# Performance work log

Hardware: AMD Instinct MI355X
Metric: run time of the kernel (lower is better)

Reference implementation:

```python
import jax, jax.numpy as jnp
import numpy as np

MARGIN = 1.0
EPS = 1e-12


def setup_inputs() -> dict:
    key = jax.random.key(0)
    k1, k2 = jax.random.split(key)
    embeddings = jax.random.normal(k1, (4096, 768), dtype=jnp.float32)
    labels = jax.random.randint(k2, (4096,), 0, 4, dtype=jnp.int64)
    return {"embeddings": embeddings, "labels": labels}


def reference(embeddings, labels):
    # F.normalize(p=2, dim=1): x / max(||x||, eps)
    norm = jnp.linalg.norm(embeddings, axis=1, keepdims=True)
    e = embeddings / jnp.maximum(norm, EPS)

    # Euclidean pairwise distance matrix (not squared)
    dot = e @ e.T                                  # [N, N]
    sq = jnp.diagonal(dot)                         # [N]
    dist = sq[None, :] - 2.0 * dot + sq[:, None]
    dist = jnp.sqrt(jnp.maximum(dist, 0.0) + EPS)  # [N, N]

    # Masks: positives = same label, off-diagonal; negatives = different label
    n = labels.shape[0]
    eq = labels[None, :] == labels[:, None]
    pos_mask = eq & ~jnp.eye(n, dtype=bool)
    neg_mask = ~eq

    # Batch-hard mining: per-anchor hardest positive (masked max) and
    # hardest negative (masked min) -- replaces the per-row Python loop.
    d_ap = jnp.max(jnp.where(pos_mask, dist, -jnp.inf), axis=1)  # [N]
    d_an = jnp.min(jnp.where(neg_mask, dist, jnp.inf), axis=1)   # [N]

    valid = jnp.any(pos_mask, axis=1)  # anchors with at least one positive
    per_anchor = jnp.maximum(d_ap - d_an + MARGIN, 0.0)
    per_anchor = jnp.where(valid, per_anchor, 0.0)
    n_valid = jnp.maximum(jnp.sum(valid.astype(jnp.float32)), 1.0)
    return jnp.sum(per_anchor) / n_valid
```

## Files before the change

### kernel.cpp

```cpp
#include <hip/hip_runtime.h>
#include <math.h>

#define N 4096
#define D 768
#define MARGIN 1.0f
#define NBLK 576

typedef _Float16 half8 __attribute__((ext_vector_type(8)));
typedef _Float16 half4 __attribute__((ext_vector_type(4)));
typedef float f32x4 __attribute__((ext_vector_type(4)));

__device__ __forceinline__ void gl2lds16(const void* g, void* l) {
    __builtin_amdgcn_global_load_lds((const __attribute__((address_space(1))) void*)g,
                                     (__attribute__((address_space(3))) void*)l, 16, 0, 0);
}

__global__ __launch_bounds__(256) void normalize_kernel(const float* __restrict__ x,
                                                        _Float16* __restrict__ e,
                                                        float* __restrict__ sq,
                                                        unsigned* __restrict__ ap_bits,
                                                        unsigned* __restrict__ an_bits,
                                                        unsigned* __restrict__ counter) {
    const int tid = threadIdx.x;
    const int wave = tid >> 6, lane = tid & 63;
    const int row = blockIdx.x * 4 + wave;

    const float4* xr = (const float4*)(x + (size_t)row * D);
    float4 f0 = xr[lane];
    float4 f1 = xr[lane + 64];
    float4 f2 = xr[lane + 128];

    float s = f0.x*f0.x + f0.y*f0.y + f0.z*f0.z + f0.w*f0.w
            + f1.x*f1.x + f1.y*f1.y + f1.z*f1.z + f1.w*f1.w
            + f2.x*f2.x + f2.y*f2.y + f2.z*f2.z + f2.w*f2.w;
    #pragma unroll
    for (int off = 1; off < 64; off <<= 1) s += __shfl_xor(s, off, 64);

    float scale = 1.0f / fmaxf(sqrtf(s), 1e-12f);

    half4* er = (half4*)(e + (size_t)row * D);
    half4 h0 = { (_Float16)(f0.x*scale), (_Float16)(f0.y*scale), (_Float16)(f0.z*scale), (_Float16)(f0.w*scale) };
    half4 h1 = { (_Float16)(f1.x*scale), (_Float16)(f1.y*scale), (_Float16)(f1.z*scale), (_Float16)(f1.w*scale) };
    half4 h2 = { (_Float16)(f2.x*scale), (_Float16)(f2.y*scale), (_Float16)(f2.z*scale), (_Float16)(f2.w*scale) };
    er[lane]       = h0;
    er[lane + 64]  = h1;
    er[lane + 128] = h2;

    if (lane == 0) {
        sq[row] = s * scale * scale;
        ap_bits[row] = 0u;
        an_bits[row] = 0x7f800000u;
    }
    if (blockIdx.x == 0 && tid == 0) *counter = 0u;
}

template<int MTN, int NTN, int BROWS>
__device__ __forceinline__ void tile_work(const _Float16* __restrict__ e,
                                          const float* __restrict__ sq,
                                          const int* __restrict__ labels,
                                          unsigned* __restrict__ ap_bits,
                                          unsigned* __restrict__ an_bits,
                                          unsigned short* S,
                                          int i0, int jbase,
                                          int wi, int wjL,
                                          int tid, int w, int lane, bool diag) {
    const int ln15 = lane & 15;
    const int lq   = lane >> 4;

    f32x4 acc[MTN][NTN] = {};

    for (int kt = 0; kt < 24; ++kt) {
        const int k0 = kt * 32;
        __syncthreads();
        #pragma unroll
        for (int p = 0; p < 2; ++p) {
            int s  = p * 256 + tid;
            int r  = s >> 2;
            int kg = (s & 3) ^ ((r >> 1) & 3);
            gl2lds16(e + (size_t)(i0 + r) * D + k0 + kg * 8,
                     (char*)S + (p * 256 + w * 64) * 16);
        }
        if constexpr (BROWS == 128) {
            #pragma unroll
            for (int p = 0; p < 2; ++p) {
                int s  = p * 256 + tid;
                int r  = s >> 2;
                int kg = (s & 3) ^ ((r >> 1) & 3);
                gl2lds16(e + (size_t)(jbase + r) * D + k0 + kg * 8,
                         (char*)S + 8192 + (p * 256 + w * 64) * 16);
            }
        } else {
            if (w < 2) {
                int s  = tid;
                int r  = s >> 2;
                int kg = (s & 3) ^ ((r >> 1) & 3);
                gl2lds16(e + (size_t)(jbase + r) * D + k0 + kg * 8,
                         (char*)S + 8192 + (w * 64) * 16);
            }
        }
        __syncthreads();

        half8 af[MTN], bf[NTN];
        #pragma unroll
        for (int mt = 0; mt < MTN; ++mt) {
            int r  = wi + mt * 16 + ln15;
            int kx = lq ^ ((r >> 1) & 3);
            af[mt] = *(const half8*)&S[r * 32 + kx * 8];
        }
        #pragma unroll
        for (int nt = 0; nt < NTN; ++nt) {
            int r  = wjL + nt * 16 + ln15;
            int kx = lq ^ ((r >> 1) & 3);
            bf[nt] = *(const half8*)&S[4096 + r * 32 + kx * 8];
        }
        #pragma unroll
        for (int mt = 0; mt < MTN; ++mt)
            #pragma unroll
            for (int nt = 0; nt < NTN; ++nt)
                acc[mt][nt] = __builtin_amdgcn_mfma_f32_16x16x32_f16(af[mt], bf[nt], acc[mt][nt], 0, 0, 0);
    }

    float sqi[MTN][4]; int labi[MTN][4];
    #pragma unroll
    for (int mt = 0; mt < MTN; ++mt)
        #pragma unroll
        for (int rg = 0; rg < 4; ++rg) {
            int i = i0 + wi + mt * 16 + lq * 4 + rg;
            sqi[mt][rg] = sq[i];
            labi[mt][rg] = labels[i];
        }
    float sqj[NTN]; int labj[NTN];
    #pragma unroll
    for (int nt = 0; nt < NTN; ++nt) {
        int j = jbase + wjL + nt * 16 + ln15;
        sqj[nt] = sq[j];
        labj[nt] = labels[j];
    }

    float api[MTN][4], ani[MTN][4], apj[NTN], anj[NTN];
    #pragma unroll
    for (int mt = 0; mt < MTN; ++mt)
        #pragma unroll
        for (int rg = 0; rg < 4; ++rg) { api[mt][rg] = -INFINITY; ani[mt][rg] = INFINITY; }
    #pragma unroll
    for (int nt = 0; nt < NTN; ++nt) { apj[nt] = -INFINITY; anj[nt] = INFINITY; }

    #pragma unroll
    for (int nt = 0; nt < NTN; ++nt) {
        int j = jbase + wjL + nt * 16 + ln15;
        #pragma unroll
        for (int mt = 0; mt < MTN; ++mt)
            #pragma unroll
            for (int rg = 0; rg < 4; ++rg) {
                int i = i0 + wi + mt * 16 + lq * 4 + rg;
                float d2 = sqi[mt][rg] + sqj[nt] - 2.0f * acc[mt][nt][rg];
                float dist = sqrtf(fmaxf(d2, 0.0f) + 1e-12f);
                if (labi[mt][rg] == labj[nt]) {
                    if (i != j) {
                        api[mt][rg] = fmaxf(api[mt][rg], dist);
                        apj[nt]     = fmaxf(apj[nt], dist);
                    }
                } else {
                    ani[mt][rg] = fminf(ani[mt][rg], dist);
                    anj[nt]     = fminf(anj[nt], dist);
                }
            }
    }

    #pragma unroll
    for (int mt = 0; mt < MTN; ++mt)
        #pragma unroll
        for (int rg = 0; rg < 4; ++rg) {
            float a_ = api[mt][rg], n_ = ani[mt][rg];
            #pragma unroll
            for (int off = 1; off < 16; off <<= 1) {
                a_ = fmaxf(a_, __shfl_xor(a_, off, 64));
                n_ = fminf(n_, __shfl_xor(n_, off, 64));
            }
            if (ln15 == 0) {
                int i = i0 + wi + mt * 16 + lq * 4 + rg;
                if (a_ > -1.0e37f) atomicMax(&ap_bits[i], __float_as_uint(a_));
                if (n_ <  1.0e37f) atomicMin(&an_bits[i], __float_as_uint(n_));
            }
        }

    if (!diag) {
        #pragma unroll
        for (int nt = 0; nt < NTN; ++nt) {
            float a_ = apj[nt], n_ = anj[nt];
            #pragma unroll
            for (int off = 16; off < 64; off <<= 1) {
                a_ = fmaxf(a_, __shfl_xor(a_, off, 64));
                n_ = fminf(n_, __shfl_xor(n_, off, 64));
            }
            if (lq == 0) {
                int j = jbase + wjL + nt * 16 + ln15;
                if (a_ > -1.0e37f) atomicMax(&ap_bits[j], __float_as_uint(a_));
                if (n_ <  1.0e37f) atomicMin(&an_bits[j], __float_as_uint(n_));
            }
        }
    }
}

__global__ __launch_bounds__(256) void mine_kernel(const _Float16* __restrict__ e,
                                                   const float* __restrict__ sq,
                                                   const int* __restrict__ labels,
                                                   unsigned* __restrict__ ap_bits,
                                                   unsigned* __restrict__ an_bits,
                                                   unsigned* __restrict__ counter,
                                                   float* __restrict__ out) {
    __shared__ unsigned short S[8192];

    const int tid  = threadIdx.x;
    const int w    = tid >> 6;
    const int lane = tid & 63;

    int t, jlo, small;
    if (blockIdx.x < 512) { t = blockIdx.x; jlo = 0; small = 0; }
    else { int s2 = blockIdx.x - 512; t = 512 + (s2 >> 2); jlo = (s2 & 3) * 32; small = 1; }

    int bi = 0, rem = t;
    while (rem >= 32 - bi) { rem -= 32 - bi; ++bi; }
    const int bj = bi + rem;
    const int i0 = bi * 128, j0 = bj * 128;

    if (!small)
        tile_work<4, 4, 128>(e, sq, labels, ap_bits, an_bits, S, i0, j0,
                             (w & 1) * 64, (w >> 1) * 64, tid, w, lane, bi == bj);
    else
        tile_work<2, 2, 32>(e, sq, labels, ap_bits, an_bits, S, i0, j0 + jlo,
                            w * 32, 0, tid, w, lane, bi == bj);

    __shared__ unsigned lastFlag;
    __syncthreads();
    if (tid == 0) {
        __builtin_amdgcn_fence(__ATOMIC_RELEASE, "agent");
        lastFlag = (atomicAdd(counter, 1u) == NBLK - 1) ? 1u : 0u;
    }
    __syncthreads();
    if (!lastFlag) return;
    __builtin_amdgcn_fence(__ATOMIC_ACQUIRE, "agent");

    __shared__ int cnt[4];
    __shared__ float red[8];
    if (tid < 4) cnt[tid] = 0;
    __syncthreads();
    int local[4] = {0, 0, 0, 0};
    for (int i = tid; i < N; i += 256) local[labels[i] & 3]++;
    #pragma unroll
    for (int c = 0; c < 4; c++) atomicAdd(&cnt[c], local[c]);
    __syncthreads();

    float sum = 0.f, nv = 0.f;
    for (int i = tid; i < N; i += 256) {
        int l = labels[i] & 3;
        if (cnt[l] >= 2) {
            nv += 1.f;
            float apv = __uint_as_float(ap_bits[i]);
            float anv = __uint_as_float(an_bits[i]);
            if (anv < 3.0e38f) sum += fmaxf(apv - anv + MARGIN, 0.f);
        }
    }

    #pragma unroll
    for (int off = 32; off; off >>= 1) {
        sum += __shfl_down(sum, off, 64);
        nv  += __shfl_down(nv,  off, 64);
    }
    if ((tid & 63) == 0) { red[tid >> 6] = sum; red[4 + (tid >> 6)] = nv; }
    __syncthreads();
    if (tid == 0) {
        float s = red[0] + red[1] + red[2] + red[3];
        float n = red[4] + red[5] + red[6] + red[7];
        out[0] = s / fmaxf(n, 1.f);
    }
}

extern "C" void kernel_launch(void* const* d_in, const int* in_sizes, int n_in,
                              void* d_out, int out_size, void* d_ws, size_t ws_size,
                              hipStream_t stream) {
    const float* x = (const float*)d_in[0];
    const int* labels = (const int*)d_in[1];
    float* out = (float*)d_out;

    _Float16* e = (_Float16*)d_ws;
    float* sq = (float*)(e + (size_t)N * D);
    unsigned* ap_bits = (unsigned*)(sq + N);
    unsigned* an_bits = ap_bits + N;
    unsigned* counter = an_bits + N;

    normalize_kernel<<<N / 4, 256, 0, stream>>>(x, e, sq, ap_bits, an_bits, counter);
    mine_kernel<<<NBLK, 256, 0, stream>>>(e, sq, labels, ap_bits, an_bits, counter, out);
}
```

Baseline: 127.3 us.

## Triple-buffer LDS K-tiles with async prefetch and remap blocks across XCDs

Replaces the single-buffered load-then-compute K loop with a three-stage LDS ring. Tiles are prefetched two steps ahead using global_load_lds, and explicit vmcnt waits replace one of the two barriers per step. It also raises wave priority around the MFMA block and remaps the block index so neighbouring tiles are spread across the eight XCDs. LDS use per block triples to 48KB, which may reduce occupancy. The small-tile path now has all four waves issue duplicate loads for the j rows so every wave's vmcnt counts line up.

```diff
diff --git a/kernel.cpp b/kernel.cpp
--- a/kernel.cpp
+++ b/kernel.cpp
@@ -5,6 +5,7 @@
 #define D 768
 #define MARGIN 1.0f
 #define NBLK 576
+#define NKT 24
 
 typedef _Float16 half8 __attribute__((ext_vector_type(8)));
 typedef _Float16 half4 __attribute__((ext_vector_type(4)));
@@ -13,6 +14,13 @@
 __device__ __forceinline__ void gl2lds16(const void* g, void* l) {
     __builtin_amdgcn_global_load_lds((const __attribute__((address_space(1))) void*)g,
                                      (__attribute__((address_space(3))) void*)l, 16, 0, 0);
+}
+
+template<int Nv>
+__device__ __forceinline__ void wait_vm() {
+    if constexpr (Nv == 0)      asm volatile("s_waitcnt vmcnt(0)" ::: "memory");
+    else if constexpr (Nv == 3) asm volatile("s_waitcnt vmcnt(3)" ::: "memory");
+    else                        asm volatile("s_waitcnt vmcnt(4)" ::: "memory");
 }
 
 __global__ __launch_bounds__(256) void normalize_kernel(const float* __restrict__ x,
@@ -52,6 +60,36 @@
         an_bits[row] = 0x7f800000u;
     }
     if (blockIdx.x == 0 && tid == 0) *counter = 0u;
+}
+
+template<int BROWS>
+__device__ __forceinline__ void stage_tile(const _Float16* __restrict__ e,
+                                           int i0, int jbase, int k0,
+                                           unsigned short* Sb, int tid, int w) {
+    #pragma unroll
+    for (int p = 0; p < 2; ++p) {
+        int s  = p * 256 + tid;
+        int r  = s >> 2;
+        int kg = (s & 3) ^ ((r >> 1) & 3);
+        gl2lds16(e + (size_t)(i0 + r) * D + k0 + kg * 8,
+                 (char*)Sb + (p * 256 + w * 64) * 16);
+    }
+    if constexpr (BROWS == 128) {
+        #pragma unroll
+        for (int p = 0; p < 2; ++p) {
+            int s  = p * 256 + tid;
+            int r  = s >> 2;
+            int kg = (s & 3) ^ ((r >> 1) & 3);
+            gl2lds16(e + (size_t)(jbase + r) * D + k0 + kg * 8,
+                     (char*)Sb + 8192 + (p * 256 + w * 64) * 16);
+        }
+    } else {
+        int s  = tid & 127;
+        int r  = s >> 2;
+        int kg = (s & 3) ^ ((r >> 1) & 3);
+        gl2lds16(e + (size_t)(jbase + r) * D + k0 + kg * 8,
+                 (char*)Sb + 8192 + ((w & 1) * 64) * 16);
+    }
 }
 
 template<int MTN, int NTN, int BROWS>
@@ -66,58 +104,47 @@
                                           int tid, int w, int lane, bool diag) {
     const int ln15 = lane & 15;
     const int lq   = lane >> 4;
+    constexpr int LPS = (BROWS == 128) ? 4 : 3;
 
     f32x4 acc[MTN][NTN] = {};
 
-    for (int kt = 0; kt < 24; ++kt) {
-        const int k0 = kt * 32;
-        __syncthreads();
-        #pragma unroll
-        for (int p = 0; p < 2; ++p) {
-            int s  = p * 256 + tid;
-            int r  = s >> 2;
-            int kg = (s & 3) ^ ((r >> 1) & 3);
-            gl2lds16(e + (size_t)(i0 + r) * D + k0 + kg * 8,
-                     (char*)S + (p * 256 + w * 64) * 16);
-        }
-        if constexpr (BROWS == 128) {
-            #pragma unroll
-            for (int p = 0; p < 2; ++p) {
-                int s  = p * 256 + tid;
-                int r  = s >> 2;
-                int kg = (s & 3) ^ ((r >> 1) & 3);
-                gl2lds16(e + (size_t)(jbase + r) * D + k0 + kg * 8,
-                         (char*)S + 8192 + (p * 256 + w * 64) * 16);
-            }
-        } else {
-            if (w < 2) {
-                int s  = tid;
-                int r  = s >> 2;
-                int kg = (s & 3) ^ ((r >> 1) & 3);
-                gl2lds16(e + (size_t)(jbase + r) * D + k0 + kg * 8,
-                         (char*)S + 8192 + (w * 64) * 16);
-            }
-        }
-        __syncthreads();
-
+    stage_tile<BROWS>(e, i0, jbase, 0,  S,        tid, w);
+    stage_tile<BROWS>(e, i0, jbase, 32, S + 8192, tid, w);
+
+    int cur = 0, nx2 = 2;
+    for (int kt = 0; kt < NKT; ++kt) {
+        if (kt < NKT - 1) wait_vm<LPS>(); else wait_vm<0>();
+        __builtin_amdgcn_s_barrier();
+        __builtin_amdgcn_sched_barrier(0);
+
+        if (kt + 2 < NKT)
+            stage_tile<BROWS>(e, i0, jbase, (kt + 2) * 32, S + nx2 * 8192, tid, w);
+        __builtin_amdgcn_sched_barrier(0);
+
+        const unsigned short* Sb = S + cur * 8192;
         half8 af[MTN], bf[NTN];
         #pragma unroll
         for (int mt = 0; mt < MTN; ++mt) {
             int r  = wi + mt * 16 + ln15;
             int kx = lq ^ ((r >> 1) & 3);
-            af[mt] = *(const half8*)&S[r * 32 + kx * 8];
+            af[mt] = *(const half8*)&Sb[r * 32 + kx * 8];
         }
         #pragma unroll
         for (int nt = 0; nt < NTN; ++nt) {
             int r  = wjL + nt * 16 + ln15;
             int kx = lq ^ ((r >> 1) & 3);
-            bf[nt] = *(const half8*)&S[4096 + r * 32 + kx * 8];
-        }
+            bf[nt] = *(const half8*)&Sb[4096 + r * 32 + kx * 8];
+        }
+        __builtin_amdgcn_s_setprio(1);
         #pragma unroll
         for (int mt = 0; mt < MTN; ++mt)
             #pragma unroll
             for (int nt = 0; nt < NTN; ++nt)
                 acc[mt][nt] = __builtin_amdgcn_mfma_f32_16x16x32_f16(af[mt], bf[nt], acc[mt][nt], 0, 0, 0);
+        __builtin_amdgcn_s_setprio(0);
+
+        cur = (cur == 2) ? 0 : cur + 1;
+        nx2 = (nx2 == 2) ? 0 : nx2 + 1;
     }
 
     float sqi[MTN][4]; int labi[MTN][4];
@@ -209,15 +236,17 @@
                                                    unsigned* __restrict__ an_bits,
                                                    unsigned* __restrict__ counter,
                                                    float* __restrict__ out) {
-    __shared__ unsigned short S[8192];
+    __shared__ unsigned short S[3 * 8192];
 
     const int tid  = threadIdx.x;
     const int w    = tid >> 6;
     const int lane = tid & 63;
 
+    const int b = (blockIdx.x % 8) * 72 + (blockIdx.x / 8);
+
     int t, jlo, small;
-    if (blockIdx.x < 512) { t = blockIdx.x; jlo = 0; small = 0; }
-    else { int s2 = blockIdx.x - 512; t = 512 + (s2 >> 2); jlo = (s2 & 3) * 32; small = 1; }
+    if (b < 512) { t = b; jlo = 0; small = 0; }
+    else { int s2 = b - 512; t = 512 + (s2 >> 2); jlo = (s2 & 3) * 32; small = 1; }
 
     int bi = 0, rem = t;
     while (rem >= 32 - bi) { rem -= 32 - bi; ++bi; }
```

After: 141.1 us. 1.11x slower.
